# Kernel tuning notes

Measured on AMD Instinct MI355X. Metric: run time of the kernel, lower is better.

The kernel has to match this reference:

```python
import jax, jax.numpy as jnp
import numpy as np

N = 100000       # nodes
E = 1600000      # edges
F_IN = 128       # num_node_features
H = 256          # graph_hidden_channels
NHID = 512
NOUT = 256
G = 256          # graphs in batch


def setup_inputs() -> dict:
    key = jax.random.key(0)
    ks = jax.random.split(key, 14)
    x = jax.random.normal(ks[0], (N, F_IN), jnp.float32)
    src = jax.random.randint(ks[1], (E,), 0, N, jnp.int32)
    dst = jax.random.randint(ks[2], (E,), 0, N, jnp.int32)
    batch = jnp.sort(jax.random.randint(ks[3], (N,), 0, G, jnp.int32))
    def lin(k, fan_in, fan_out):
        return jax.random.normal(k, (fan_in, fan_out), jnp.float32) * (1.0 / np.sqrt(fan_in))
    return {
        "x": x, "src": src, "dst": dst, "batch": batch,
        "W1": lin(ks[4], F_IN, H), "b1": jnp.zeros((H,), jnp.float32),
        "W2": lin(ks[5], H, H),    "b2": jnp.zeros((H,), jnp.float32),
        "W3": lin(ks[6], H, H),    "b3": jnp.zeros((H,), jnp.float32),
        "Wm1": lin(ks[7], H, NHID), "bm1": jnp.zeros((NHID,), jnp.float32),
        "Wm2": lin(ks[8], NHID, NOUT), "bm2": jnp.zeros((NOUT,), jnp.float32),
    }


def _gcn_layer(h_in, W, b, src, dst, dinv):
    # GCNConv: transform, then symmetric-normalized aggregation with self-loops.
    h = h_in @ W                                            # [N, out]
    norm = (dinv[src] * dinv[dst])[:, None]                 # [E, 1]
    agg = jax.ops.segment_sum(h[src] * norm, dst, num_segments=N)
    agg = agg + h * (dinv * dinv)[:, None]                  # self-loop term (norm = 1/deg)
    return agg + b


def reference(x, src, dst, batch, W1, b1, W2, b2, W3, b3, Wm1, bm1, Wm2, bm2):
    # degrees include the added self-loop (+1)
    deg = 1.0 + jax.ops.segment_sum(jnp.ones((E,), x.dtype), dst, num_segments=N)
    dinv = jax.lax.rsqrt(deg)                               # deg^{-1/2}

    h = jax.nn.relu(_gcn_layer(x, W1, b1, src, dst, dinv))
    h = jax.nn.relu(_gcn_layer(h, W2, b2, src, dst, dinv))
    h = _gcn_layer(h, W3, b3, src, dst, dinv)               # no relu before pooling

    # global mean pool over graphs
    counts = jax.ops.segment_sum(jnp.ones((N,), x.dtype), batch, num_segments=G)
    pooled = jax.ops.segment_sum(h, batch, num_segments=G) / jnp.maximum(counts, 1.0)[:, None]

    out = jax.nn.relu(pooled @ Wm1 + bm1) @ Wm2 + bm2       # [G, NOUT]
    return out
```

## Files before the change

kernel.cpp:

```cpp
#include <hip/hip_runtime.h>
#include <hip/hip_bf16.h>

#define N_NODES 100000
#define N_EDGES 1600000
#define F_IN    128
#define H       256
#define NHID    512
#define NOUT    256
#define G_GR    256

typedef unsigned short u16;
typedef __attribute__((ext_vector_type(8))) short s16x8;
typedef __attribute__((ext_vector_type(8))) unsigned short u16x8;
typedef __attribute__((ext_vector_type(4))) float f32x4;

__device__ __forceinline__ float bf2f(u16 u) {
    union { unsigned int i; float f; } v; v.i = ((unsigned int)u) << 16; return v.f;
}
__device__ __forceinline__ u16 f2bf(float f) {
    union { float f; unsigned int i; } v; v.f = f;
    unsigned int x = v.i;
    x += 0x7fffu + ((x >> 16) & 1u);
    return (u16)(x >> 16);
}

#define CD_BLKS   1563
#define SPX_BLKS  ((N_NODES * F_IN) / 1024)
#define T1_BLKS   ((F_IN * H) / 256)
#define T2_BLKS   ((H * H) / 256)
#define T3_BLKS   ((H * H) / 256)
#define TM1_BLKS  ((H * NHID) / 256)
#define TM2_BLKS  ((NHID * NOUT) / 256)
#define HEAD_BLKS (CD_BLKS + T1_BLKS + T2_BLKS + T3_BLKS + TM1_BLKS + TM2_BLKS + 2)

__device__ __forceinline__ void transpose_split_body(const float* __restrict__ W,
        u16* __restrict__ thi, u16* __restrict__ tlo, int K, int N, int id) {
    int n = id / K, k = id - n * K;
    float f = W[(size_t)k * N + n];
    u16 h = f2bf(f);
    thi[id] = h;
    tlo[id] = f2bf(f - bf2f(h));
}

__global__ __launch_bounds__(256) void prep_head(
        const int* __restrict__ dst, int* __restrict__ degc,
        const float* __restrict__ W1, u16* __restrict__ t1h, u16* __restrict__ t1l,
        const float* __restrict__ W2, u16* __restrict__ t2h, u16* __restrict__ t2l,
        const float* __restrict__ W3, u16* __restrict__ t3h, u16* __restrict__ t3l,
        const float* __restrict__ Wm1, u16* __restrict__ tm1h, u16* __restrict__ tm1l,
        const float* __restrict__ Wm2, u16* __restrict__ tm2h, u16* __restrict__ tm2l,
        const int* __restrict__ batch, int* __restrict__ goff) {
    int bid = blockIdx.x;
    if (bid < CD_BLKS) {
        int base = bid * 1024 + threadIdx.x;
#pragma unroll
        for (int q = 0; q < 4; q++) {
            int e = base + q * 256;
            if (e < N_EDGES) atomicAdd(&degc[dst[e]], 1);
        }
        return;
    }
    bid -= CD_BLKS;
    if (bid < T1_BLKS) {
        transpose_split_body(W1, t1h, t1l, F_IN, H, bid * 256 + threadIdx.x);
        return;
    }
    bid -= T1_BLKS;
    if (bid < T2_BLKS) {
        transpose_split_body(W2, t2h, t2l, H, H, bid * 256 + threadIdx.x);
        return;
    }
    bid -= T2_BLKS;
    if (bid < T3_BLKS) {
        transpose_split_body(W3, t3h, t3l, H, H, bid * 256 + threadIdx.x);
        return;
    }
    bid -= T3_BLKS;
    if (bid < TM1_BLKS) {
        transpose_split_body(Wm1, tm1h, tm1l, H, NHID, bid * 256 + threadIdx.x);
        return;
    }
    bid -= TM1_BLKS;
    if (bid < TM2_BLKS) {
        transpose_split_body(Wm2, tm2h, tm2l, NHID, NOUT, bid * 256 + threadIdx.x);
        return;
    }
    bid -= TM2_BLKS;
    {
        int g = bid * 256 + threadIdx.x;
        if (g > G_GR) return;
        int lo = 0, hi = N_NODES;
        while (lo < hi) {
            int mid = (lo + hi) >> 1;
            if (batch[mid] < g) lo = mid + 1; else hi = mid;
        }
        goff[g] = lo;
    }
}

__global__ void scan_partial(const int* __restrict__ cnt, int* __restrict__ partial) {
    __shared__ int s[256];
    int t = threadIdx.x;
    int i = blockIdx.x * 256 + t;
    int v = (i < N_NODES) ? cnt[i] : 0;
    s[t] = v; __syncthreads();
    for (int off = 128; off > 0; off >>= 1) {
        if (t < off) s[t] += s[t + off];
        __syncthreads();
    }
    if (t == 0) partial[blockIdx.x] = s[0];
}

__global__ void scan_offsets(int* __restrict__ partial, int nb, int* __restrict__ rowp) {
    __shared__ int s[512];
    int t = threadIdx.x;
    int orig = (t < nb) ? partial[t] : 0;
    s[t] = orig; __syncthreads();
    for (int off = 1; off < 512; off <<= 1) {
        int u = (t >= off) ? s[t - off] : 0;
        __syncthreads();
        s[t] += u;
        __syncthreads();
    }
    if (t < nb) partial[t] = s[t] - orig;
    if (t == 0) rowp[N_NODES] = N_EDGES;
}

__global__ void scan_final_dinv(const int* __restrict__ cnt, const int* __restrict__ partial,
                                int* __restrict__ rowp, int* __restrict__ cur,
                                float* __restrict__ dinv) {
    __shared__ int s[256];
    int t = threadIdx.x;
    int i = blockIdx.x * 256 + t;
    int v = (i < N_NODES) ? cnt[i] : 0;
    s[t] = v; __syncthreads();
    for (int off = 1; off < 256; off <<= 1) {
        int u = (t >= off) ? s[t - off] : 0;
        __syncthreads();
        s[t] += u;
        __syncthreads();
    }
    if (i < N_NODES) {
        int r = partial[blockIdx.x] + s[t] - v;
        rowp[i] = r;
        cur[i] = r;
        dinv[i] = rsqrtf(1.0f + (float)v);
    }
}

__global__ __launch_bounds__(256) void scatter_splitx(
        const int* __restrict__ src, const int* __restrict__ dst,
        const float* __restrict__ dinv, int* __restrict__ cur,
        int2* __restrict__ ep,
        const float* __restrict__ x, u16* __restrict__ x_bf) {
    int bid = blockIdx.x;
    if (bid < CD_BLKS) {
        int base = bid * 1024 + threadIdx.x;
#pragma unroll
        for (int q = 0; q < 4; q++) {
            int e = base + q * 256;
            if (e < N_EDGES) {
                int d = dst[e];
                int s = src[e];
                float w = dinv[d] * dinv[s];
                int pos = atomicAdd(&cur[d], 1);
                int2 v; v.x = s; v.y = __float_as_int(w);
                ep[pos] = v;
            }
        }
        return;
    }
    bid -= CD_BLKS;
    {
        int idx = bid * 256 + threadIdx.x;
        float4 f = *(const float4*)&x[(size_t)idx * 4];
        ushort4 o;
        o.x = f2bf(f.x); o.y = f2bf(f.y); o.z = f2bf(f.z); o.w = f2bf(f.w);
        *(ushort4*)&x_bf[(size_t)idx * 4] = o;
    }
}

__global__ __launch_bounds__(256) void gcn_agg256(
        const u16* __restrict__ in, const int* __restrict__ rowp,
        const int2* __restrict__ ep, const float* __restrict__ dinv,
        u16* __restrict__ outp) {
    int node = blockIdx.x * 8 + (threadIdx.x >> 5);
    int l = threadIdx.x & 31;
    int beg = rowp[node], end = rowp[node + 1];
    float a[8] = {};
    int e = beg;
    int2 pr[8];
    bool have = (e + 8 <= end);
    if (have) {
#pragma unroll
        for (int q = 0; q < 8; q++) pr[q] = ep[e + q];
    }
    while (have) {
        int2 g8[8];
#pragma unroll
        for (int q = 0; q < 8; q++) g8[q] = pr[q];
        int en = e + 8;
        bool haven = (en + 8 <= end);
        if (haven) {
#pragma unroll
            for (int q = 0; q < 8; q++) pr[q] = ep[en + q];
        }
#pragma unroll
        for (int q = 0; q < 8; q++) {
            u16x8 u = *(const u16x8*)&in[(size_t)g8[q].x * H + l * 8];
            float wt = __int_as_float(g8[q].y);
#pragma unroll
            for (int r = 0; r < 8; r++) a[r] += bf2f(u[r]) * wt;
        }
        e = en; have = haven;
    }
    for (; e < end; e++) {
        int2 pe = ep[e];
        float wt = __int_as_float(pe.y);
        u16x8 u = *(const u16x8*)&in[(size_t)pe.x * H + l * 8];
#pragma unroll
        for (int r = 0; r < 8; r++) a[r] += bf2f(u[r]) * wt;
    }
    float di = dinv[node];
    u16x8 us = *(const u16x8*)&in[(size_t)node * H + l * 8];
    float dd = di * di;
    u16x8 o;
#pragma unroll
    for (int r = 0; r < 8; r++) o[r] = f2bf(a[r] + bf2f(us[r]) * dd);
    *(u16x8*)&outp[(size_t)node * H + l * 8] = o;
}

__global__ __launch_bounds__(256) void gcn_agg128(
        const u16* __restrict__ in, const int* __restrict__ rowp,
        const int2* __restrict__ ep, const float* __restrict__ dinv,
        u16* __restrict__ outp) {
    int node = blockIdx.x * 16 + (threadIdx.x >> 4);
    int l = threadIdx.x & 15;
    int beg = rowp[node], end = rowp[node + 1];
    float a[8] = {};
    int e = beg;
    int2 pr[8];
    bool have = (e + 8 <= end);
    if (have) {
#pragma unroll
        for (int q = 0; q < 8; q++) pr[q] = ep[e + q];
    }
    while (have) {
        int2 g8[8];
#pragma unroll
        for (int q = 0; q < 8; q++) g8[q] = pr[q];
        int en = e + 8;
        bool haven = (en + 8 <= end);
        if (haven) {
#pragma unroll
            for (int q = 0; q < 8; q++) pr[q] = ep[en + q];
        }
#pragma unroll
        for (int q = 0; q < 8; q++) {
            u16x8 u = *(const u16x8*)&in[(size_t)g8[q].x * F_IN + l * 8];
            float wt = __int_as_float(g8[q].y);
#pragma unroll
            for (int r = 0; r < 8; r++) a[r] += bf2f(u[r]) * wt;
        }
        e = en; have = haven;
    }
    for (; e < end; e++) {
        int2 pe = ep[e];
        float wt = __int_as_float(pe.y);
        u16x8 u = *(const u16x8*)&in[(size_t)pe.x * F_IN + l * 8];
#pragma unroll
        for (int r = 0; r < 8; r++) a[r] += bf2f(u[r]) * wt;
    }
    float di = dinv[node];
    u16x8 us = *(const u16x8*)&in[(size_t)node * F_IN + l * 8];
    float dd = di * di;
    u16x8 o;
#pragma unroll
    for (int r = 0; r < 8; r++) o[r] = f2bf(a[r] + bf2f(us[r]) * dd);
    *(u16x8*)&outp[(size_t)node * F_IN + l * 8] = o;
}

template<int K, bool RELU>
__global__ __launch_bounds__(256) void gemm_bias(
        const u16* __restrict__ A,
        const u16* __restrict__ Bhi, const u16* __restrict__ Blo,
        const float* __restrict__ bias, u16* __restrict__ C, int M) {
    __shared__ __align__(16) u16 sA[128 * 40];
    __shared__ __align__(16) u16 sB[2 * 128 * 40];
    const int tid = threadIdx.x;
    const int w = tid >> 6, l = tid & 63;
    const int wm = (w & 1) * 64, wn = (w >> 1) * 64;
    const int bm = blockIdx.x * 128, bn = blockIdx.y * 128;
    const int srow = tid >> 2;
    const int schunk = (tid & 3) * 8;
    const int lr = l & 15, lg = (l >> 4) * 8;

    f32x4 acc[4][4] = {};

    for (int k0 = 0; k0 < K; k0 += 32) {
        {
            int r0 = bm + srow, r1 = bm + srow + 64;
            u16x8 v0 = {}, v1 = {};
            if (r0 < M) v0 = *(const u16x8*)&A[(size_t)r0 * K + k0 + schunk];
            if (r1 < M) v1 = *(const u16x8*)&A[(size_t)r1 * K + k0 + schunk];
            *(u16x8*)&sA[srow * 40 + schunk] = v0;
            *(u16x8*)&sA[(srow + 64) * 40 + schunk] = v1;
        }
        {
            int n0 = bn + srow, n1 = bn + srow + 64;
            *(u16x8*)&sB[srow * 40 + schunk] = *(const u16x8*)&Bhi[(size_t)n0 * K + k0 + schunk];
            *(u16x8*)&sB[(srow + 64) * 40 + schunk] = *(const u16x8*)&Bhi[(size_t)n1 * K + k0 + schunk];
            *(u16x8*)&sB[128 * 40 + srow * 40 + schunk] = *(const u16x8*)&Blo[(size_t)n0 * K + k0 + schunk];
            *(u16x8*)&sB[128 * 40 + (srow + 64) * 40 + schunk] = *(const u16x8*)&Blo[(size_t)n1 * K + k0 + schunk];
        }
        __syncthreads();

        s16x8 af[4], bh[4], bl[4];
#pragma unroll
        for (int i = 0; i < 4; i++)
            af[i] = __builtin_bit_cast(s16x8, *(const u16x8*)&sA[(wm + i * 16 + lr) * 40 + lg]);
#pragma unroll
        for (int j = 0; j < 4; j++) {
            bh[j] = __builtin_bit_cast(s16x8, *(const u16x8*)&sB[(wn + j * 16 + lr) * 40 + lg]);
            bl[j] = __builtin_bit_cast(s16x8, *(const u16x8*)&sB[128 * 40 + (wn + j * 16 + lr) * 40 + lg]);
        }
#pragma unroll
        for (int i = 0; i < 4; i++) {
#pragma unroll
            for (int j = 0; j < 4; j++) {
                acc[i][j] = __builtin_amdgcn_mfma_f32_16x16x32_bf16(af[i], bh[j], acc[i][j], 0, 0, 0);
                acc[i][j] = __builtin_amdgcn_mfma_f32_16x16x32_bf16(af[i], bl[j], acc[i][j], 0, 0, 0);
            }
        }
        __syncthreads();
    }

    float bcol[4];
#pragma unroll
    for (int j = 0; j < 4; j++) bcol[j] = bias[bn + wn + j * 16 + lr];

    const int lq = (l >> 4) * 4;
#pragma unroll
    for (int i = 0; i < 4; i++) {
#pragma unroll
        for (int r0 = 0; r0 < 4; r0++) {
            int row = bm + wm + i * 16 + lq + r0;
            if (row < M) {
#pragma unroll
                for (int j = 0; j < 4; j++) {
                    float v = acc[i][j][r0] + bcol[j];
                    if (RELU) v = fmaxf(v, 0.f);
                    C[(size_t)row * H + bn + wn + j * 16 + lr] = f2bf(v);
                }
            }
        }
    }
}

template<int K, int NW, bool RELU, bool F32OUT>
__global__ __launch_bounds__(256) void gemm_split(
        const u16* __restrict__ Ahi, const u16* __restrict__ Alo,
        const u16* __restrict__ Bhi, const u16* __restrict__ Blo,
        const float* __restrict__ bias,
        u16* __restrict__ Chi, u16* __restrict__ Clo, float* __restrict__ Cf,
        int M) {
    __shared__ __align__(16) u16 sA[2 * 128 * 40];
    __shared__ __align__(16) u16 sB[2 * 128 * 40];
    const int tid = threadIdx.x;
    const int w = tid >> 6, l = tid & 63;
    const int wm = (w & 1) * 64, wn = (w >> 1) * 64;
    const int bm = blockIdx.x * 128, bn = blockIdx.y * 128;
    const int srow = tid >> 2;
    const int schunk = (tid & 3) * 8;
    const int lr = l & 15, lg = (l >> 4) * 8;

    f32x4 acc[4][4] = {};

    for (int k0 = 0; k0 < K; k0 += 32) {
        {
            int r0 = bm + srow, r1 = bm + srow + 64;
            u16x8 v0 = {}, v1 = {}, w0 = {}, w1 = {};
            if (r0 < M) {
                v0 = *(const u16x8*)&Ahi[(size_t)r0 * K + k0 + schunk];
                w0 = *(const u16x8*)&Alo[(size_t)r0 * K + k0 + schunk];
            }
            if (r1 < M) {
                v1 = *(const u16x8*)&Ahi[(size_t)r1 * K + k0 + schunk];
                w1 = *(const u16x8*)&Alo[(size_t)r1 * K + k0 + schunk];
            }
            *(u16x8*)&sA[srow * 40 + schunk] = v0;
            *(u16x8*)&sA[(srow + 64) * 40 + schunk] = v1;
            *(u16x8*)&sA[128 * 40 + srow * 40 + schunk] = w0;
            *(u16x8*)&sA[128 * 40 + (srow + 64) * 40 + schunk] = w1;
        }
        {
            int n0 = bn + srow, n1 = bn + srow + 64;
            *(u16x8*)&sB[srow * 40 + schunk] = *(const u16x8*)&Bhi[(size_t)n0 * K + k0 + schunk];
            *(u16x8*)&sB[(srow + 64) * 40 + schunk] = *(const u16x8*)&Bhi[(size_t)n1 * K + k0 + schunk];
            *(u16x8*)&sB[128 * 40 + srow * 40 + schunk] = *(const u16x8*)&Blo[(size_t)n0 * K + k0 + schunk];
            *(u16x8*)&sB[128 * 40 + (srow + 64) * 40 + schunk] = *(const u16x8*)&Blo[(size_t)n1 * K + k0 + schunk];
        }
        __syncthreads();

        s16x8 af[4], al[4], bh[4], bl[4];
#pragma unroll
        for (int i = 0; i < 4; i++) {
            af[i] = __builtin_bit_cast(s16x8, *(const u16x8*)&sA[(wm + i * 16 + lr) * 40 + lg]);
            al[i] = __builtin_bit_cast(s16x8, *(const u16x8*)&sA[128 * 40 + (wm + i * 16 + lr) * 40 + lg]);
        }
#pragma unroll
        for (int j = 0; j < 4; j++) {
            bh[j] = __builtin_bit_cast(s16x8, *(const u16x8*)&sB[(wn + j * 16 + lr) * 40 + lg]);
            bl[j] = __builtin_bit_cast(s16x8, *(const u16x8*)&sB[128 * 40 + (wn + j * 16 + lr) * 40 + lg]);
        }
#pragma unroll
        for (int i = 0; i < 4; i++) {
#pragma unroll
            for (int j = 0; j < 4; j++) {
                acc[i][j] = __builtin_amdgcn_mfma_f32_16x16x32_bf16(af[i], bh[j], acc[i][j], 0, 0, 0);
                acc[i][j] = __builtin_amdgcn_mfma_f32_16x16x32_bf16(af[i], bl[j], acc[i][j], 0, 0, 0);
                acc[i][j] = __builtin_amdgcn_mfma_f32_16x16x32_bf16(al[i], bh[j], acc[i][j], 0, 0, 0);
            }
        }
        __syncthreads();
    }

    float bcol[4];
#pragma unroll
    for (int j = 0; j < 4; j++) bcol[j] = bias[bn + wn + j * 16 + lr];

    const int lq = (l >> 4) * 4;
#pragma unroll
    for (int i = 0; i < 4; i++) {
#pragma unroll
        for (int r0 = 0; r0 < 4; r0++) {
            int row = bm + wm + i * 16 + lq + r0;
            if (row < M) {
#pragma unroll
                for (int j = 0; j < 4; j++) {
                    float v = acc[i][j][r0] + bcol[j];
                    if (RELU) v = fmaxf(v, 0.f);
                    size_t idx = (size_t)row * NW + bn + wn + j * 16 + lr;
                    if (F32OUT) {
                        Cf[idx] = v;
                    } else {
                        u16 hv = f2bf(v);
                        Chi[idx] = hv;
                        Clo[idx] = f2bf(v - bf2f(hv));
                    }
                }
            }
        }
    }
}

__global__ __launch_bounds__(256) void pool_split(
        const u16* __restrict__ a3, const int* __restrict__ goff,
        u16* __restrict__ phi, u16* __restrict__ plo) {
    int g = blockIdx.x, t = threadIdx.x;
    int beg = goff[g], end = goff[g + 1];
    float acc = 0.f;
    int i = beg;
    for (; i + 4 <= end; i += 4) {
        float v0 = bf2f(a3[(size_t)(i + 0) * H + t]);
        float v1 = bf2f(a3[(size_t)(i + 1) * H + t]);
        float v2 = bf2f(a3[(size_t)(i + 2) * H + t]);
        float v3 = bf2f(a3[(size_t)(i + 3) * H + t]);
        acc += (v0 + v1) + (v2 + v3);
    }
    for (; i < end; i++) acc += bf2f(a3[(size_t)i * H + t]);
    acc /= fmaxf((float)(end - beg), 1.f);
    u16 hv = f2bf(acc);
    phi[g * H + t] = hv;
    plo[g * H + t] = f2bf(acc - bf2f(hv));
}

extern "C" void kernel_launch(void* const* d_in, const int* in_sizes, int n_in,
                              void* d_out, int out_size, void* d_ws, size_t ws_size,
                              hipStream_t stream) {
    const float* x   = (const float*)d_in[0];
    const int*   src = (const int*)d_in[1];
    const int*   dst = (const int*)d_in[2];
    const int*   bat = (const int*)d_in[3];
    const float* W1  = (const float*)d_in[4];  const float* b1  = (const float*)d_in[5];
    const float* W2  = (const float*)d_in[6];  const float* b2  = (const float*)d_in[7];
    const float* W3  = (const float*)d_in[8];  const float* b3  = (const float*)d_in[9];
    const float* Wm1 = (const float*)d_in[10]; const float* bm1 = (const float*)d_in[11];
    const float* Wm2 = (const float*)d_in[12]; const float* bm2 = (const float*)d_in[13];
    float* out = (float*)d_out;

    char* p = (char*)d_ws;
    auto carve = [&](size_t bytes) -> void* {
        void* r = (void*)p;
        p += (bytes + 511) & ~(size_t)511;
        return r;
    };
    u16*   x_bf    = (u16*)  carve((size_t)N_NODES * F_IN * 2);
    u16*   aggX    = (u16*)  carve((size_t)N_NODES * F_IN * 2);
    u16*   bufA    = (u16*)  carve((size_t)N_NODES * H * 2);
    u16*   bufB    = (u16*)  carve((size_t)N_NODES * H * 2);
    float* dinv    = (float*)carve((size_t)N_NODES * 4);
    int*   degc    = (int*)  carve((size_t)N_NODES * 4);
    int*   rowp    = (int*)  carve((size_t)(N_NODES + 1) * 4);
    int*   cur     = (int*)  carve((size_t)N_NODES * 4);
    int2*  ep      = (int2*) carve((size_t)N_EDGES * 8);
    int*   partial = (int*)  carve(4096);
    int*   goff    = (int*)  carve((size_t)(G_GR + 1) * 4);
    u16*   Wt1_hi  = (u16*)  carve((size_t)F_IN * H * 2);
    u16*   Wt1_lo  = (u16*)  carve((size_t)F_IN * H * 2);
    u16*   Wt2_hi  = (u16*)  carve((size_t)H * H * 2);
    u16*   Wt2_lo  = (u16*)  carve((size_t)H * H * 2);
    u16*   Wt3_hi  = (u16*)  carve((size_t)H * H * 2);
    u16*   Wt3_lo  = (u16*)  carve((size_t)H * H * 2);
    u16*   Wm1t_hi = (u16*)  carve((size_t)H * NHID * 2);
    u16*   Wm1t_lo = (u16*)  carve((size_t)H * NHID * 2);
    u16*   Wm2t_hi = (u16*)  carve((size_t)NHID * NOUT * 2);
    u16*   Wm2t_lo = (u16*)  carve((size_t)NHID * NOUT * 2);
    u16*   p_hi    = (u16*)  carve((size_t)G_GR * H * 2);
    u16*   p_lo    = (u16*)  carve((size_t)G_GR * H * 2);
    u16*   y_hi    = (u16*)  carve((size_t)G_GR * H * 2);
    u16*   y_lo    = (u16*)  carve((size_t)G_GR * H * 2);
    u16*   hd_hi   = (u16*)  carve((size_t)G_GR * NHID * 2);
    u16*   hd_lo   = (u16*)  carve((size_t)G_GR * NHID * 2);

    const int NB = (N_NODES + 255) / 256;

    hipMemsetAsync(degc, 0, (size_t)N_NODES * 4, stream);
    prep_head<<<HEAD_BLKS, 256, 0, stream>>>(dst, degc,
                                             W1, Wt1_hi, Wt1_lo,
                                             W2, Wt2_hi, Wt2_lo,
                                             W3, Wt3_hi, Wt3_lo,
                                             Wm1, Wm1t_hi, Wm1t_lo,
                                             Wm2, Wm2t_hi, Wm2t_lo, bat, goff);
    scan_partial<<<NB, 256, 0, stream>>>(degc, partial);
    scan_offsets<<<1, 512, 0, stream>>>(partial, NB, rowp);
    scan_final_dinv<<<NB, 256, 0, stream>>>(degc, partial, rowp, cur, dinv);
    scatter_splitx<<<CD_BLKS + SPX_BLKS, 256, 0, stream>>>(src, dst, dinv, cur, ep, x, x_bf);

    dim3 ggrid((N_NODES + 127) / 128, 2);

    gcn_agg128<<<N_NODES / 16, 256, 0, stream>>>(x_bf, rowp, ep, dinv, aggX);
    gemm_bias<F_IN, true><<<ggrid, 256, 0, stream>>>(aggX, Wt1_hi, Wt1_lo, b1, bufA, N_NODES);
    gcn_agg256<<<N_NODES / 8, 256, 0, stream>>>(bufA, rowp, ep, dinv, bufB);
    gemm_bias<H, true><<<ggrid, 256, 0, stream>>>(bufB, Wt2_hi, Wt2_lo, b2, bufA, N_NODES);
    gcn_agg256<<<N_NODES / 8, 256, 0, stream>>>(bufA, rowp, ep, dinv, bufB);

    pool_split<<<G_GR, 256, 0, stream>>>(bufB, goff, p_hi, p_lo);
    dim3 g3(2, 2), gm1(2, 4), gm2(2, 2);
    gemm_split<H, H, false, false><<<g3, 256, 0, stream>>>(
        p_hi, p_lo, Wt3_hi, Wt3_lo, b3, y_hi, y_lo, nullptr, G_GR);
    gemm_split<H, NHID, true, false><<<gm1, 256, 0, stream>>>(
        y_hi, y_lo, Wm1t_hi, Wm1t_lo, bm1, hd_hi, hd_lo, nullptr, G_GR);
    gemm_split<NHID, NOUT, false, true><<<gm2, 256, 0, stream>>>(
        hd_hi, hd_lo, Wm2t_hi, Wm2t_lo, bm2, nullptr, nullptr, out, G_GR);
}
```

Baseline: 747.4 us.

## Fuse final GCN aggregation with mean-pool via block-reduced atomics

```diff
diff --git a/kernel.cpp b/kernel.cpp
--- a/kernel.cpp
+++ b/kernel.cpp
@@ -278,6 +278,90 @@
 #pragma unroll
     for (int r = 0; r < 8; r++) o[r] = f2bf(a[r] + bf2f(us[r]) * dd);
     *(u16x8*)&outp[(size_t)node * F_IN + l * 8] = o;
+}
+
+__global__ __launch_bounds__(256) void gcn_agg_pool(
+        const u16* __restrict__ in, const int* __restrict__ rowp,
+        const int2* __restrict__ ep, const float* __restrict__ dinv,
+        const int* __restrict__ batch, float* __restrict__ poolacc) {
+    __shared__ __align__(16) float pacc[8][H];
+    __shared__ int gslot[8];
+    const int tid = threadIdx.x;
+    const int hw = tid >> 5;
+    const int l = tid & 31;
+    const int node = blockIdx.x * 8 + hw;
+    const int gbase = batch[blockIdx.x * 8];
+
+    int beg = rowp[node], end = rowp[node + 1];
+    float a[8] = {};
+    int e = beg;
+    int2 pr[8];
+    bool have = (e + 8 <= end);
+    if (have) {
+#pragma unroll
+        for (int q = 0; q < 8; q++) pr[q] = ep[e + q];
+    }
+    while (have) {
+        int2 g8[8];
+#pragma unroll
+        for (int q = 0; q < 8; q++) g8[q] = pr[q];
+        int en = e + 8;
+        bool haven = (en + 8 <= end);
+        if (haven) {
+#pragma unroll
+            for (int q = 0; q < 8; q++) pr[q] = ep[en + q];
+        }
+#pragma unroll
+        for (int q = 0; q < 8; q++) {
+            u16x8 u = *(const u16x8*)&in[(size_t)g8[q].x * H + l * 8];
+            float wt = __int_as_float(g8[q].y);
+#pragma unroll
+            for (int r = 0; r < 8; r++) a[r] += bf2f(u[r]) * wt;
+        }
+        e = en; have = haven;
+    }
+    for (; e < end; e++) {
+        int2 pe = ep[e];
+        float wt = __int_as_float(pe.y);
+        u16x8 u = *(const u16x8*)&in[(size_t)pe.x * H + l * 8];
+#pragma unroll
+        for (int r = 0; r < 8; r++) a[r] += bf2f(u[r]) * wt;
+    }
+    float di = dinv[node];
+    u16x8 us = *(const u16x8*)&in[(size_t)node * H + l * 8];
+    float dd = di * di;
+    f32x4 lo4, hi4;
+#pragma unroll
+    for (int r = 0; r < 4; r++) lo4[r] = a[r] + bf2f(us[r]) * dd;
+#pragma unroll
+    for (int r = 0; r < 4; r++) hi4[r] = a[r + 4] + bf2f(us[r + 4]) * dd;
+    *(f32x4*)&pacc[hw][l * 8] = lo4;
+    *(f32x4*)&pacc[hw][l * 8 + 4] = hi4;
+    if (l == 0) gslot[hw] = batch[node] - gbase;
+    __syncthreads();
+
+    int smax = gslot[7];
+    float v[8];
+#pragma unroll
+    for (int q = 0; q < 8; q++) v[q] = pacc[q][tid];
+    for (int s = 0; s <= smax; s++) {
+        float acc = 0.f;
+#pragma unroll
+        for (int q = 0; q < 8; q++)
+            if (gslot[q] == s) acc += v[q];
+        atomicAdd(&poolacc[(size_t)(gbase + s) * H + tid], acc);
+    }
+}
+
+__global__ __launch_bounds__(256) void pool_finalize2(
+        const float* __restrict__ poolacc, const int* __restrict__ goff,
+        u16* __restrict__ phi, u16* __restrict__ plo) {
+    int g = blockIdx.x, t = threadIdx.x;
+    float c = (float)(goff[g + 1] - goff[g]);
+    float acc = poolacc[(size_t)g * H + t] / fmaxf(c, 1.f);
+    u16 hv = f2bf(acc);
+    phi[g * H + t] = hv;
+    plo[g * H + t] = f2bf(acc - bf2f(hv));
 }
 
 template<int K, bool RELU>
@@ -452,27 +536,6 @@
             }
         }
     }
-}
-
-__global__ __launch_bounds__(256) void pool_split(
-        const u16* __restrict__ a3, const int* __restrict__ goff,
-        u16* __restrict__ phi, u16* __restrict__ plo) {
-    int g = blockIdx.x, t = threadIdx.x;
-    int beg = goff[g], end = goff[g + 1];
-    float acc = 0.f;
-    int i = beg;
-    for (; i + 4 <= end; i += 4) {
-        float v0 = bf2f(a3[(size_t)(i + 0) * H + t]);
-        float v1 = bf2f(a3[(size_t)(i + 1) * H + t]);
-        float v2 = bf2f(a3[(size_t)(i + 2) * H + t]);
-        float v3 = bf2f(a3[(size_t)(i + 3) * H + t]);
-        acc += (v0 + v1) + (v2 + v3);
-    }
-    for (; i < end; i++) acc += bf2f(a3[(size_t)i * H + t]);
-    acc /= fmaxf((float)(end - beg), 1.f);
-    u16 hv = f2bf(acc);
-    phi[g * H + t] = hv;
-    plo[g * H + t] = f2bf(acc - bf2f(hv));
 }
 
 extern "C" void kernel_launch(void* const* d_in, const int* in_sizes, int n_in,
@@ -522,10 +585,12 @@
     u16*   y_lo    = (u16*)  carve((size_t)G_GR * H * 2);
     u16*   hd_hi   = (u16*)  carve((size_t)G_GR * NHID * 2);
     u16*   hd_lo   = (u16*)  carve((size_t)G_GR * NHID * 2);
+    float* poolacc = (float*)carve((size_t)G_GR * H * 4);
 
     const int NB = (N_NODES + 255) / 256;
 
     hipMemsetAsync(degc, 0, (size_t)N_NODES * 4, stream);
+    hipMemsetAsync(poolacc, 0, (size_t)G_GR * H * 4, stream);
     prep_head<<<HEAD_BLKS, 256, 0, stream>>>(dst, degc,
                                              W1, Wt1_hi, Wt1_lo,
                                              W2, Wt2_hi, Wt2_lo,
@@ -543,9 +608,9 @@
     gemm_bias<F_IN, true><<<ggrid, 256, 0, stream>>>(aggX, Wt1_hi, Wt1_lo, b1, bufA, N_NODES);
     gcn_agg256<<<N_NODES / 8, 256, 0, stream>>>(bufA, rowp, ep, dinv, bufB);
     gemm_bias<H, true><<<ggrid, 256, 0, stream>>>(bufB, Wt2_hi, Wt2_lo, b2, bufA, N_NODES);
-    gcn_agg256<<<N_NODES / 8, 256, 0, stream>>>(bufA, rowp, ep, dinv, bufB);
-
-    pool_split<<<G_GR, 256, 0, stream>>>(bufB, goff, p_hi, p_lo);
+    gcn_agg_pool<<<N_NODES / 8, 256, 0, stream>>>(bufA, rowp, ep, dinv, bat, poolacc);
+    pool_finalize2<<<G_GR, 256, 0, stream>>>(poolacc, goff, p_hi, p_lo);
+
     dim3 g3(2, 2), gm1(2, 4), gm2(2, 2);
     gemm_split<H, H, false, false><<<g3, 256, 0, stream>>>(
         p_hi, p_lo, Wt3_hi, Wt3_lo, b3, y_hi, y_lo, nullptr, G_GR);
```

Result: faster. 724.4 us (-3.1%).
